# Performance work log

Hardware: AMD Instinct MI355X
Metric: run time of the kernel (lower is better)

The kernel has to match this reference:

```python
import jax, jax.numpy as jnp
import numpy as np

B, NFIELD, NEMB, NFILTER, NLAYERS = 256, 64, 64, 128, 3


def setup_inputs() -> dict:
    key = jax.random.key(0)
    ks = jax.random.split(key, 5)
    x = jax.random.normal(ks[0], (B, NFIELD, NEMB), dtype=jnp.float32)
    # Conv1d(k=1, bias=False) weights, squeezed to (out_ch, in_ch). Small init for stability.
    W0 = jax.random.normal(ks[1], (NFILTER, NFIELD * NFIELD), dtype=jnp.float32) * 0.02
    W1 = jax.random.normal(ks[2], (NFILTER, NFIELD * NFILTER), dtype=jnp.float32) * 0.02
    W2 = jax.random.normal(ks[3], (NFILTER, NFIELD * NFILTER), dtype=jnp.float32) * 0.02
    Wa = jax.random.normal(ks[4], (1, NLAYERS * NFILTER), dtype=jnp.float32) * 0.02
    return {"x": x, "W0": W0, "W1": W1, "W2": W2, "Wa": Wa}


def reference(x, W0, W1, W2, Wa):
    # x: (B, F, E). CIN recurrence over a fixed small number of layers.
    Ws = [W0, W1, W2]
    x0 = x
    xk = x
    pooled = []
    for W in Ws:
        # outer product over field axes: (B, F, C, E)
        h = x0[:, :, None, :] * xk[:, None, :, :]
        b, f, c, e = h.shape
        h = h.reshape(b, f * c, e)
        # 1x1 conv == GEMM over channel dim, then ReLU
        xk = jax.nn.relu(jnp.einsum('oc,bce->boe', W, h))
        # sum-pool over embedding dim: (B, nfilter)
        pooled.append(jnp.sum(xk, axis=-1))
    feats = jnp.concatenate(pooled, axis=1)  # (B, nlayers*nfilter)
    y = feats @ Wa.T                         # (B, 1)
    return y[:, 0]
```

## Files before the change

### kernel.cpp

```cpp
#include <hip/hip_runtime.h>

#define NBATCH 256

typedef __attribute__((ext_vector_type(8))) short bf16x8;
typedef __attribute__((ext_vector_type(4))) float f32x4;

__device__ __forceinline__ unsigned short f2b(float f) {
    unsigned u = __float_as_uint(f);
    u = (u + 0x7fffu + ((u >> 16) & 1u)) >> 16;
    return (unsigned short)u;
}
__device__ __forceinline__ float b2f(unsigned short h) {
    return __uint_as_float(((unsigned)h) << 16);
}
__device__ __forceinline__ void async16(const void* g, void* l) {
    __builtin_amdgcn_global_load_lds((const __attribute__((address_space(1))) unsigned int*)g,
                                     (__attribute__((address_space(3))) unsigned int*)l, 16, 0, 0);
}

__global__ void prep_all(const float* __restrict__ x,
                         const float* __restrict__ W0,
                         const float* __restrict__ W1,
                         const float* __restrict__ W2,
                         unsigned short* __restrict__ x0t,
                         unsigned short* __restrict__ x0f,
                         unsigned short* __restrict__ Wp0,
                         unsigned short* __restrict__ Wp1,
                         unsigned short* __restrict__ Wp2)
{
    const int bid = blockIdx.x, tid = threadIdx.x;
    if (bid < 2560) {
        const float* W; unsigned short* Wp; int CLOG, KLOG, lbid;
        if (bid < 512)       { W = W0; Wp = Wp0; CLOG = 6; KLOG = 12; lbid = bid; }
        else if (bid < 1536) { W = W1; Wp = Wp1; CLOG = 7; KLOG = 13; lbid = bid - 512; }
        else                 { W = W2; Wp = Wp2; CLOG = 7; KLOG = 13; lbid = bid - 1536; }
        const int base = (lbid * 256 + tid) * 4;
        int o = base >> KLOG, k = base & ((1 << KLOG) - 1);
        int f = k >> CLOG, c = k & ((1 << CLOG) - 1);
        int rg = o >> 4, l15 = o & 15;
        int cs = c >> 5, kseg = (c >> 3) & 3, j = c & 7;
        int NCS = 1 << (CLOG - 5);
        int NK = 64 * NCS;
        int kstep = f * NCS + cs;
        size_t dst = (((size_t)rg * NK + kstep) * 64 + kseg * 16 + l15) * 8 + j;
        const float4 wv = *(const float4*)(W + base);
        *(ushort4*)(Wp + dst) = make_ushort4(f2b(wv.x), f2b(wv.y), f2b(wv.z), f2b(wv.w));
    } else {
        const int base = ((bid - 2560) * 256 + tid) * 4;
        int b = base >> 12, r = base & 4095, f = r >> 6, e0 = r & 63;
        const float4 xv = *(const float4*)(x + base);
        ushort4 v = make_ushort4(f2b(xv.x), f2b(xv.y), f2b(xv.z), f2b(xv.w));
        *(ushort4*)(x0f + b * 4096 + f * 64 + e0) = v;
        x0t[b * 4096 + (e0 + 0) * 64 + f] = v.x;
        x0t[b * 4096 + (e0 + 1) * 64 + f] = v.y;
        x0t[b * 4096 + (e0 + 2) * 64 + f] = v.z;
        x0t[b * 4096 + (e0 + 3) * 64 + f] = v.w;
    }
}

template <int CL, bool LAST>
__global__ __launch_bounds__(512, 2) void layer_k(
    const unsigned short* __restrict__ Wp,
    const unsigned short* __restrict__ Bsrc,
    const unsigned short* __restrict__ x0f,
    const float* __restrict__ Wa_l,
    unsigned short* __restrict__ xknext,
    float* __restrict__ ybuf)
{
    constexpr int NCS  = CL / 32;
    constexpr int NCS2 = NCS / 2;
    constexpr int NK   = 64 * NCS;
    __shared__ char sm[49152];
    char* smX = sm;
    char* smR = sm + 32768;

    const int bid = blockIdx.x, tid = threadIdx.x;
    const int rg = bid & 7, sgg = bid >> 3;
    const int lane = tid & 63, w = tid >> 6;
    const int p = w & 3, kg = w >> 2;
    const int s = sgg * 4 + p;
    const int l15 = lane & 15, kseg = lane >> 4;

#pragma unroll
    for (int q = 0; q < 4; ++q)
        async16((const char*)x0f + (size_t)(sgg * 4 + q) * 8192 + w * 1024 + lane * 16,
                smX + q * 8192 + w * 1024);

    bf16x8 bq[NCS2][4];
    {
        const char* Bb = (const char*)Bsrc + (size_t)s * (CL * 128) + kseg * 16;
#pragma unroll
        for (int i = 0; i < NCS2; ++i)
#pragma unroll
            for (int nt = 0; nt < 4; ++nt)
                bq[i][nt] = *(const bf16x8*)(Bb + (nt * 16 + l15) * (CL * 2)
                                             + (kg * NCS2 + i) * 64);
    }

    const char* Ag = (const char*)Wp + (size_t)rg * NK * 1024 + (kseg * 16 + l15) * 16;
#define LD_A(dst, f) { _Pragma("unroll") for (int i_ = 0; i_ < NCS2; ++i_) \
    dst[i_] = *(const bf16x8*)(Ag + (size_t)((f) * NCS + kg * NCS2 + i_) * 1024); }

    bf16x8 aqA[NCS2], aqB[NCS2];
    LD_A(aqA, 0);

    __syncthreads();

    const unsigned short* XS = (const unsigned short*)(smX + p * 8192);
    const f32x4 ZERO = {0.f, 0.f, 0.f, 0.f};
    f32x4 acc[4], accf[4];
#pragma unroll
    for (int nt = 0; nt < 4; ++nt) acc[nt] = ZERO;

#define CONSUME(A, f) { \
    const float sv0 = b2f(XS[(f) * 64 + l15]); \
    const float sv1 = b2f(XS[(f) * 64 + 16 + l15]); \
    const float sv2 = b2f(XS[(f) * 64 + 32 + l15]); \
    const float sv3 = b2f(XS[(f) * 64 + 48 + l15]); \
    _Pragma("unroll") for (int i_ = 0; i_ < NCS2; ++i_) { \
        _Pragma("unroll") for (int nt_ = 0; nt_ < 4; ++nt_) \
            accf[nt_] = __builtin_amdgcn_mfma_f32_16x16x32_bf16( \
                A[i_], bq[i_][nt_], (i_ == 0) ? ZERO : accf[nt_], 0, 0, 0); \
    } \
    acc[0] += accf[0] * f32x4{sv0, sv0, sv0, sv0}; \
    acc[1] += accf[1] * f32x4{sv1, sv1, sv1, sv1}; \
    acc[2] += accf[2] * f32x4{sv2, sv2, sv2, sv2}; \
    acc[3] += accf[3] * f32x4{sv3, sv3, sv3, sv3}; }

    for (int ch = 0; ch < 8; ++ch) {
#pragma unroll
        for (int i = 0; i < NCS2; ++i)
            asm volatile("" :: "v"(bq[i][0]), "v"(bq[i][1]), "v"(bq[i][2]), "v"(bq[i][3]));
#pragma unroll
        for (int fi = 0; fi < 8; ++fi) {
            const int f = ch * 8 + fi;
            if ((fi & 1) == 0) {
                LD_A(aqB, f + 1);
                CONSUME(aqA, f);
            } else {
                if (f < 63) LD_A(aqA, f + 1);
                CONSUME(aqB, f);
            }
        }
    }
#undef LD_A
#undef CONSUME

    if (kg == 1) {
#pragma unroll
        for (int nt = 0; nt < 4; ++nt)
            *(f32x4*)(smR + p * 4096 + lane * 64 + nt * 16) = acc[nt];
    }
    __syncthreads();
    if (kg == 0) {
#pragma unroll
        for (int nt = 0; nt < 4; ++nt)
            acc[nt] += *(const f32x4*)(smR + p * 4096 + lane * 64 + nt * 16);

        const float4 wa = *(const float4*)(Wa_l + rg * 16 + kseg * 4);
        float ypart = 0.f;
#pragma unroll
        for (int nt = 0; nt < 4; ++nt) {
            f32x4 v = acc[nt];
            v.x = fmaxf(v.x, 0.f); v.y = fmaxf(v.y, 0.f);
            v.z = fmaxf(v.z, 0.f); v.w = fmaxf(v.w, 0.f);
            ypart = fmaf(wa.x, v.x, ypart);
            ypart = fmaf(wa.y, v.y, ypart);
            ypart = fmaf(wa.z, v.z, ypart);
            ypart = fmaf(wa.w, v.w, ypart);
            if (!LAST) {
                unsigned lo = (unsigned)f2b(v.x) | ((unsigned)f2b(v.y) << 16);
                unsigned hi = (unsigned)f2b(v.z) | ((unsigned)f2b(v.w) << 16);
                *(uint2*)((char*)xknext + (size_t)s * 16384 + (nt * 16 + l15) * 256
                          + (rg * 16 + kseg * 4) * 2) = make_uint2(lo, hi);
            }
        }
#pragma unroll
        for (int off = 32; off >= 1; off >>= 1)
            ypart += __shfl_down(ypart, off, 64);
        if (lane == 0) ybuf[s * 8 + rg] = ypart;
    }
}

__global__ void finalize_k(const float* __restrict__ ybuf, float* __restrict__ y) {
    const int b = threadIdx.x;
    float sum = 0.f;
#pragma unroll
    for (int l = 0; l < 3; ++l)
#pragma unroll
        for (int r = 0; r < 8; ++r)
            sum += ybuf[l * 2048 + b * 8 + r];
    y[b] = sum;
}

extern "C" void kernel_launch(void* const* d_in, const int* in_sizes, int n_in,
                              void* d_out, int out_size, void* d_ws, size_t ws_size,
                              hipStream_t stream) {
    const float* x  = (const float*)d_in[0];
    const float* W0 = (const float*)d_in[1];
    const float* W1 = (const float*)d_in[2];
    const float* W2 = (const float*)d_in[3];
    const float* Wa = (const float*)d_in[4];
    float* y = (float*)d_out;

    char* ws = (char*)d_ws;
    unsigned short* Wp0  = (unsigned short*)(ws + 0x000000);
    unsigned short* Wp1  = (unsigned short*)(ws + 0x110000);
    unsigned short* Wp2  = (unsigned short*)(ws + 0x320000);
    unsigned short* x0t  = (unsigned short*)(ws + 0x530000);
    unsigned short* x0f  = (unsigned short*)(ws + 0x730000);
    unsigned short* xkA  = (unsigned short*)(ws + 0x930000);
    unsigned short* xkB  = (unsigned short*)(ws + 0xD30000);
    float*          ybuf = (float*)(ws + 0x1130000);

    hipLaunchKernelGGL(prep_all, dim3(3584), dim3(256), 0, stream,
                       x, W0, W1, W2, x0t, x0f, Wp0, Wp1, Wp2);

    hipLaunchKernelGGL((layer_k<64, false>), dim3(512), dim3(512), 0, stream,
                       Wp0, x0t, x0f, Wa + 0, xkA, ybuf + 0);
    hipLaunchKernelGGL((layer_k<128, false>), dim3(512), dim3(512), 0, stream,
                       Wp1, xkA, x0f, Wa + 128, xkB, ybuf + 2048);
    hipLaunchKernelGGL((layer_k<128, true>), dim3(512), dim3(512), 0, stream,
                       Wp2, xkB, x0f, Wa + 256, xkA, ybuf + 4096);

    hipLaunchKernelGGL(finalize_k, dim3(1), dim3(256), 0, stream, ybuf, y);
}
```

Before: 109.5 us.

## Stage weight tiles through double-buffered LDS and pack x0 scale loads

The A-operand weight tiles are no longer loaded straight from global memory into registers with a software prefetch. They are now staged through LDS with async global-to-LDS copies, double-buffered per 16-kstep chunk with a barrier per chunk, so all eight waves share each weight load. The x0 scaling values are repacked in prep so that the four per-lane scale factors arrive in one 8-byte LDS read. In exchange, LDS use per block rises to 64KB, which may limit occupancy, and the per-chunk barriers add synchronisation.

```diff
diff --git a/kernel.cpp b/kernel.cpp
--- a/kernel.cpp
+++ b/kernel.cpp
@@ -9,9 +9,6 @@
     unsigned u = __float_as_uint(f);
     u = (u + 0x7fffu + ((u >> 16) & 1u)) >> 16;
     return (unsigned short)u;
-}
-__device__ __forceinline__ float b2f(unsigned short h) {
-    return __uint_as_float(((unsigned)h) << 16);
 }
 __device__ __forceinline__ void async16(const void* g, void* l) {
     __builtin_amdgcn_global_load_lds((const __attribute__((address_space(1))) unsigned int*)g,
@@ -23,7 +20,7 @@
                          const float* __restrict__ W1,
                          const float* __restrict__ W2,
                          unsigned short* __restrict__ x0t,
-                         unsigned short* __restrict__ x0f,
+                         unsigned short* __restrict__ x0fp,
                          unsigned short* __restrict__ Wp0,
                          unsigned short* __restrict__ Wp1,
                          unsigned short* __restrict__ Wp2)
@@ -50,7 +47,12 @@
         int b = base >> 12, r = base & 4095, f = r >> 6, e0 = r & 63;
         const float4 xv = *(const float4*)(x + base);
         ushort4 v = make_ushort4(f2b(xv.x), f2b(xv.y), f2b(xv.z), f2b(xv.w));
-        *(ushort4*)(x0f + b * 4096 + f * 64 + e0) = v;
+        unsigned short* xp = x0fp + b * 4096 + f * 64;
+        const int hi = e0 >> 4;
+        xp[((e0 + 0) & 15) * 4 + hi] = v.x;
+        xp[((e0 + 1) & 15) * 4 + hi] = v.y;
+        xp[((e0 + 2) & 15) * 4 + hi] = v.z;
+        xp[((e0 + 3) & 15) * 4 + hi] = v.w;
         x0t[b * 4096 + (e0 + 0) * 64 + f] = v.x;
         x0t[b * 4096 + (e0 + 1) * 64 + f] = v.y;
         x0t[b * 4096 + (e0 + 2) * 64 + f] = v.z;
@@ -62,7 +64,7 @@
 __global__ __launch_bounds__(512, 2) void layer_k(
     const unsigned short* __restrict__ Wp,
     const unsigned short* __restrict__ Bsrc,
-    const unsigned short* __restrict__ x0f,
+    const unsigned short* __restrict__ x0fp,
     const float* __restrict__ Wa_l,
     unsigned short* __restrict__ xknext,
     float* __restrict__ ybuf)
@@ -70,9 +72,11 @@
     constexpr int NCS  = CL / 32;
     constexpr int NCS2 = NCS / 2;
     constexpr int NK   = 64 * NCS;
-    __shared__ char sm[49152];
-    char* smX = sm;
-    char* smR = sm + 32768;
+    constexpr int NCH  = NK / 16;
+    constexpr int FPC  = 16 / NCS;
+    __shared__ char sm[65536];
+    char* smA = sm;
+    char* smX = sm + 32768;
 
     const int bid = blockIdx.x, tid = threadIdx.x;
     const int rg = bid & 7, sgg = bid >> 3;
@@ -83,7 +87,7 @@
 
 #pragma unroll
     for (int q = 0; q < 4; ++q)
-        async16((const char*)x0f + (size_t)(sgg * 4 + q) * 8192 + w * 1024 + lane * 16,
+        async16((const char*)x0fp + (size_t)(sgg * 4 + q) * 8192 + w * 1024 + lane * 16,
                 smX + q * 8192 + w * 1024);
 
     bf16x8 bq[NCS2][4];
@@ -97,13 +101,14 @@
                                              + (kg * NCS2 + i) * 64);
     }
 
-    const char* Ag = (const char*)Wp + (size_t)rg * NK * 1024 + (kseg * 16 + l15) * 16;
-#define LD_A(dst, f) { _Pragma("unroll") for (int i_ = 0; i_ < NCS2; ++i_) \
-    dst[i_] = *(const bf16x8*)(Ag + (size_t)((f) * NCS + kg * NCS2 + i_) * 1024); }
-
-    bf16x8 aqA[NCS2], aqB[NCS2];
-    LD_A(aqA, 0);
-
+    const char* Ab = (const char*)Wp + (size_t)rg * NK * 1024;
+    auto stage = [&](int ch, int buf) {
+        const char* src = Ab + ((size_t)ch * 16 + w * 2) * 1024 + lane * 16;
+        char* dst = smA + buf * 16384 + w * 2048;
+        async16(src, dst);
+        async16(src + 1024, dst + 1024);
+    };
+    stage(0, 0);
     __syncthreads();
 
     const unsigned short* XS = (const unsigned short*)(smX + p * 8192);
@@ -112,50 +117,49 @@
 #pragma unroll
     for (int nt = 0; nt < 4; ++nt) acc[nt] = ZERO;
 
-#define CONSUME(A, f) { \
-    const float sv0 = b2f(XS[(f) * 64 + l15]); \
-    const float sv1 = b2f(XS[(f) * 64 + 16 + l15]); \
-    const float sv2 = b2f(XS[(f) * 64 + 32 + l15]); \
-    const float sv3 = b2f(XS[(f) * 64 + 48 + l15]); \
-    _Pragma("unroll") for (int i_ = 0; i_ < NCS2; ++i_) { \
-        _Pragma("unroll") for (int nt_ = 0; nt_ < 4; ++nt_) \
-            accf[nt_] = __builtin_amdgcn_mfma_f32_16x16x32_bf16( \
-                A[i_], bq[i_][nt_], (i_ == 0) ? ZERO : accf[nt_], 0, 0, 0); \
-    } \
-    acc[0] += accf[0] * f32x4{sv0, sv0, sv0, sv0}; \
-    acc[1] += accf[1] * f32x4{sv1, sv1, sv1, sv1}; \
-    acc[2] += accf[2] * f32x4{sv2, sv2, sv2, sv2}; \
-    acc[3] += accf[3] * f32x4{sv3, sv3, sv3, sv3}; }
-
-    for (int ch = 0; ch < 8; ++ch) {
+    for (int ch = 0; ch < NCH; ++ch) {
+        const int cur = ch & 1;
+        if (ch + 1 < NCH) stage(ch + 1, cur ^ 1);
 #pragma unroll
         for (int i = 0; i < NCS2; ++i)
             asm volatile("" :: "v"(bq[i][0]), "v"(bq[i][1]), "v"(bq[i][2]), "v"(bq[i][3]));
-#pragma unroll
-        for (int fi = 0; fi < 8; ++fi) {
-            const int f = ch * 8 + fi;
-            if ((fi & 1) == 0) {
-                LD_A(aqB, f + 1);
-                CONSUME(aqA, f);
-            } else {
-                if (f < 63) LD_A(aqA, f + 1);
-                CONSUME(aqB, f);
-            }
+        const char* Abuf = smA + cur * 16384 + lane * 16;
+#pragma unroll
+        for (int fi = 0; fi < FPC; ++fi) {
+            const int f = ch * FPC + fi;
+            const uint2 sp = *(const uint2*)(XS + f * 64 + l15 * 4);
+            const float sv0 = __uint_as_float(sp.x << 16);
+            const float sv1 = __uint_as_float(sp.x & 0xffff0000u);
+            const float sv2 = __uint_as_float(sp.y << 16);
+            const float sv3 = __uint_as_float(sp.y & 0xffff0000u);
+            bf16x8 a[NCS2];
+#pragma unroll
+            for (int i = 0; i < NCS2; ++i)
+                a[i] = *(const bf16x8*)(Abuf + (fi * NCS + kg * NCS2 + i) * 1024);
+#pragma unroll
+            for (int i = 0; i < NCS2; ++i)
+#pragma unroll
+                for (int nt = 0; nt < 4; ++nt)
+                    accf[nt] = __builtin_amdgcn_mfma_f32_16x16x32_bf16(
+                        a[i], bq[i][nt], (i == 0) ? ZERO : accf[nt], 0, 0, 0);
+            acc[0] += accf[0] * f32x4{sv0, sv0, sv0, sv0};
+            acc[1] += accf[1] * f32x4{sv1, sv1, sv1, sv1};
+            acc[2] += accf[2] * f32x4{sv2, sv2, sv2, sv2};
+            acc[3] += accf[3] * f32x4{sv3, sv3, sv3, sv3};
         }
-    }
-#undef LD_A
-#undef CONSUME
+        __syncthreads();
+    }
 
     if (kg == 1) {
 #pragma unroll
         for (int nt = 0; nt < 4; ++nt)
-            *(f32x4*)(smR + p * 4096 + lane * 64 + nt * 16) = acc[nt];
+            *(f32x4*)(smA + p * 4096 + lane * 64 + nt * 16) = acc[nt];
     }
     __syncthreads();
     if (kg == 0) {
 #pragma unroll
         for (int nt = 0; nt < 4; ++nt)
-            acc[nt] += *(const f32x4*)(smR + p * 4096 + lane * 64 + nt * 16);
+            acc[nt] += *(const f32x4*)(smA + p * 4096 + lane * 64 + nt * 16);
 
         const float4 wa = *(const float4*)(Wa_l + rg * 16 + kseg * 4);
         float ypart = 0.f;
@@ -208,20 +212,20 @@
     unsigned short* Wp1  = (unsigned short*)(ws + 0x110000);
     unsigned short* Wp2  = (unsigned short*)(ws + 0x320000);
     unsigned short* x0t  = (unsigned short*)(ws + 0x530000);
-    unsigned short* x0f  = (unsigned short*)(ws + 0x730000);
+    unsigned short* x0fp = (unsigned short*)(ws + 0x730000);
     unsigned short* xkA  = (unsigned short*)(ws + 0x930000);
     unsigned short* xkB  = (unsigned short*)(ws + 0xD30000);
     float*          ybuf = (float*)(ws + 0x1130000);
 
     hipLaunchKernelGGL(prep_all, dim3(3584), dim3(256), 0, stream,
-                       x, W0, W1, W2, x0t, x0f, Wp0, Wp1, Wp2);
+                       x, W0, W1, W2, x0t, x0fp, Wp0, Wp1, Wp2);
 
     hipLaunchKernelGGL((layer_k<64, false>), dim3(512), dim3(512), 0, stream,
-                       Wp0, x0t, x0f, Wa + 0, xkA, ybuf + 0);
+                       Wp0, x0t, x0fp, Wa + 0, xkA, ybuf + 0);
     hipLaunchKernelGGL((layer_k<128, false>), dim3(512), dim3(512), 0, stream,
-                       Wp1, xkA, x0f, Wa + 128, xkB, ybuf + 2048);
+                       Wp1, xkA, x0fp, Wa + 128, xkB, ybuf + 2048);
     hipLaunchKernelGGL((layer_k<128, true>), dim3(512), dim3(512), 0, stream,
-                       Wp2, xkB, x0f, Wa + 256, xkA, ybuf + 4096);
+                       Wp2, xkB, x0fp, Wa + 256, xkA, ybuf + 4096);
 
     hipLaunchKernelGGL(finalize_k, dim3(1), dim3(256), 0, stream, ybuf, y);
 }
```

Result: no change. 109.7 us (+0.2%).
